# Optimization experiments

Hardware: AMD Instinct MI355X
Metric: run time of the kernel (lower is better)

The kernel has to match this reference:

```python
import jax, jax.numpy as jnp
import numpy as np

B, C, W, H = 8, 256, 64, 64
C8 = C // 8


def setup_inputs() -> dict:
    key = jax.random.key(0)
    ks = jax.random.split(key, 8)
    # xavier_uniform for 1x1 convs: bound = sqrt(6/(fan_in+fan_out))
    def xavier(k, out_c, in_c):
        bound = np.sqrt(6.0 / (in_c + out_c))
        return jax.random.uniform(k, (out_c, in_c), jnp.float32, -bound, bound)
    return {
        "x": jax.random.normal(ks[0], (B, C, W, H), jnp.float32),
        "Wf": xavier(ks[1], C8, C),
        "bf": jnp.zeros((C8,), jnp.float32),
        "Wg": xavier(ks[2], C8, C),
        "bg": jnp.zeros((C8,), jnp.float32),
        "Wh": xavier(ks[3], C, C),
        "bh": jnp.zeros((C,), jnp.float32),
        "gamma": jnp.zeros((1,), jnp.float32),
    }


def reference(x, Wf, bf, Wg, bg, Wh, bh, gamma):
    b, c, w, h = x.shape
    n = w * h
    xf = x.reshape(b, c, n)                                   # (B, C, N)
    # 1x1 convs == per-position channel GEMMs
    f = jnp.einsum('oc,bcn->bon', Wf, xf) + bf[None, :, None]  # (B, C/8, N)
    g = jnp.einsum('oc,bcn->bon', Wg, xf) + bg[None, :, None]  # (B, C/8, N)
    hh = jnp.einsum('oc,bcn->bon', Wh, xf) + bh[None, :, None] # (B, C, N)
    # attention[b,i,j] = softmax_j( f[b,:,i] . g[b,:,j] )
    att = jax.nn.softmax(jnp.einsum('boi,boj->bij', f, g), axis=-1)
    # torch.bmm(h, attention): out[b,c,i] = sum_k h[b,c,k] * att[b,k,i]
    sa = jnp.einsum('bck,bki->bci', hh, att).reshape(b, c, w, h)
    return gamma * sa + x
```

## Files before the change

kernel.cpp:

```cpp
#include <hip/hip_runtime.h>
#include <hip/hip_bf16.h>

#define BB 8
#define CC 256
#define NN 4096
#define LOG2E 1.44269504088896340736f
#define SHIFT 48.0f

typedef __attribute__((ext_vector_type(8))) short short8;
typedef __attribute__((ext_vector_type(4))) float f32x4;

static __device__ __forceinline__ unsigned short f2b(float x) {
  __hip_bfloat16 h = __float2bfloat16(x);
  return *reinterpret_cast<unsigned short*>(&h);
}
static __device__ __forceinline__ unsigned int pk2(float a, float b) {
  return (unsigned int)f2b(a) | ((unsigned int)f2b(b) << 16);
}


__global__ __launch_bounds__(256) void k_wprep(
    const float* __restrict__ Wf, const float* __restrict__ bfv,
    const float* __restrict__ Wg, const float* __restrict__ bgv,
    const float* __restrict__ Wh, const float* __restrict__ bhv,
    unsigned short* __restrict__ wA, float* __restrict__ ball)
{
  const int t = threadIdx.x;
  const int fi = blockIdx.x * 4 + (t >> 6);
  const int l = t & 63;
  const int mg = fi >> 3, kg = fi & 7;
  const int o = mg * 16 + (l & 15);
  const int c0 = kg * 32 + (l >> 4) * 8;
  const float* src; float scale = 1.0f;
  if (o < 32)      { src = Wf + (size_t)o * CC; scale = LOG2E; }
  else if (o < 64) { src = Wg + (size_t)(o - 32) * CC; }
  else             { src = Wh + (size_t)(o - 64) * CC; }
  float4 a = *(const float4*)(src + c0);
  float4 c = *(const float4*)(src + c0 + 4);
  short8 v;
  v[0] = (short)f2b(a.x * scale); v[1] = (short)f2b(a.y * scale);
  v[2] = (short)f2b(a.z * scale); v[3] = (short)f2b(a.w * scale);
  v[4] = (short)f2b(c.x * scale); v[5] = (short)f2b(c.y * scale);
  v[6] = (short)f2b(c.z * scale); v[7] = (short)f2b(c.w * scale);
  *(short8*)(wA + (size_t)fi * 512 + l * 8) = v;
  if (blockIdx.x == 0 && t < 320)
    ball[t] = (t < 32) ? bfv[t] * LOG2E : (t < 64) ? bgv[t - 32] : bhv[t - 64];
}

__global__ __launch_bounds__(512) void k_fgh(
    const float* __restrict__ x, const unsigned short* __restrict__ wA,
    const float* __restrict__ ball,
    unsigned short* __restrict__ fA, unsigned short* __restrict__ gB,
    unsigned short* __restrict__ hA)
{
  __shared__ __align__(16) char smem[41984];
  unsigned short* xb = (unsigned short*)smem;
  unsigned short* TL = (unsigned short*)smem;
  const int bid = blockIdx.x;
  const int b = bid & 7, i0 = (bid >> 3) * 64;
  const int t = threadIdx.x, w = t >> 6, l = t & 63;
  const int ig_w = w & 3, mg0 = (w >> 2) * 10;
  f32x4 acc[10] = {};
  for (int cc = 0; cc < 4; ++cc) {
    __syncthreads();
    {
      short8 v;
      const float* xp = x + ((size_t)b * CC + cc * 64 + w * 8) * NN + i0 + l;
      #pragma unroll
      for (int e = 0; e < 8; ++e) v[e] = (short)f2b(xp[(size_t)e * NN]);
      int frag = (w >> 2) * 4 + (l >> 4);
      int lp = (w & 3) * 16 + (l & 15);
      *(short8*)(xb + (frag * 64 + lp) * 8) = v;
    }
    __syncthreads();
    #pragma unroll
    for (int kg2 = 0; kg2 < 2; ++kg2) {
      short8 bfrag = *(const short8*)(xb + ((kg2 * 4 + ig_w) * 64 + l) * 8);
      int kg = cc * 2 + kg2;
      #pragma unroll
      for (int j = 0; j < 10; ++j) {
        short8 afrag = *(const short8*)(wA +
            ((size_t)((mg0 + j) * 8 + kg)) * 512 + l * 8);
        acc[j] = __builtin_amdgcn_mfma_f32_16x16x32_bf16(afrag, bfrag, acc[j], 0, 0, 0);
      }
    }
  }
  __syncthreads();
  #pragma unroll
  for (int j = 0; j < 10; ++j) {
    int ob = (mg0 + j) * 16 + (l >> 4) * 4;
    float4 bl = *(const float4*)(ball + ob);
    int irow = ig_w * 16 + (l & 15);
    ushort4 pv;
    pv.x = f2b(acc[j][0] + bl.x); pv.y = f2b(acc[j][1] + bl.y);
    pv.z = f2b(acc[j][2] + bl.z); pv.w = f2b(acc[j][3] + bl.w);
    *(ushort4*)(TL + irow * 328 + ob) = pv;
  }
  __syncthreads();
  if (t < 256) {
    int kg_p = t >> 6;
    int o8 = (l >> 4) * 8;
    int irow = kg_p * 16 + (l & 15);
    short8 vf = *(const short8*)(TL + irow * 328 + o8);
    short8 vg = *(const short8*)(TL + irow * 328 + 32 + o8);
    size_t kgG = (size_t)b * 256 + (i0 >> 4) + kg_p;
    *(short8*)(fA + kgG * 512 + l * 8) = vf;
    *(short8*)(gB + kgG * 512 + l * 8) = vg;
  }
  #pragma unroll
  for (int q = 0; q < 4; ++q) {
    int slot = t + q * 512;
    int fr = slot >> 6, ll = slot & 63;
    int cg = fr >> 1, kcl = fr & 1;
    int orow = 64 + cg * 16 + (ll & 15);
    int pbase = kcl * 32 + (ll >> 4) * 8;
    short8 v;
    #pragma unroll
    for (int e = 0; e < 8; ++e) v[e] = (short)TL[(pbase + e) * 328 + orow];
    size_t idx = (((size_t)b * 16 + cg) * 128 + (i0 >> 5) + kcl) * 512 + ll * 8;
    *(short8*)(hA + idx) = v;
  }
}

__global__ __launch_bounds__(512) void k_stats(
    const unsigned short* __restrict__ fA, const unsigned short* __restrict__ gB,
    float* __restrict__ cshift)
{
  __shared__ __align__(16) unsigned short sg[2][16 * 512];
  const int bid = blockIdx.x;
  const int b = bid & 7, kt = bid >> 3;
  const int t = threadIdx.x, w = t >> 6, l = t & 63;
  const int li = l & 15, lh = l >> 4;
  short8 af = *(const short8*)(fA + ((size_t)b * 256 + kt * 8 + w) * 512 + l * 8);
  const unsigned short* gb = gB + (size_t)b * 256 * 512;
  f32x4 zero = {0.f, 0.f, 0.f, 0.f};
  {
    uint4 v0 = *(const uint4*)(gb + ((size_t)(w * 2 + 0) * 64 + l) * 8);
    uint4 v1 = *(const uint4*)(gb + ((size_t)(w * 2 + 1) * 64 + l) * 8);
    *(uint4*)(&sg[0][((w * 2 + 0) * 64 + l) * 8]) = v0;
    *(uint4*)(&sg[0][((w * 2 + 1) * 64 + l) * 8]) = v1;
  }
  __syncthreads();
  float s[4] = {0.f, 0.f, 0.f, 0.f};
  for (int jt = 0; jt < 16; ++jt) {
    if (jt < 15) {
      uint4 v0 = *(const uint4*)(gb + ((size_t)((jt + 1) * 16 + w * 2 + 0) * 64 + l) * 8);
      uint4 v1 = *(const uint4*)(gb + ((size_t)((jt + 1) * 16 + w * 2 + 1) * 64 + l) * 8);
      unsigned short* dst = &sg[(jt + 1) & 1][0];
      *(uint4*)(dst + ((w * 2 + 0) * 64 + l) * 8) = v0;
      *(uint4*)(dst + ((w * 2 + 1) * 64 + l) * 8) = v1;
    }
    const unsigned short* src = &sg[jt & 1][0];
    #pragma unroll
    for (int jf = 0; jf < 16; ++jf) {
      short8 bfrag = *(const short8*)(src + (jf * 64 + l) * 8);
      f32x4 d = __builtin_amdgcn_mfma_f32_16x16x32_bf16(af, bfrag, zero, 0, 0, 0);
      s[0] += exp2f(d[0] - SHIFT);
      s[1] += exp2f(d[1] - SHIFT);
      s[2] += exp2f(d[2] - SHIFT);
      s[3] += exp2f(d[3] - SHIFT);
    }
    __syncthreads();
  }
  #pragma unroll
  for (int mk = 1; mk < 16; mk <<= 1)
    #pragma unroll
    for (int r = 0; r < 4; ++r) s[r] += __shfl_xor(s[r], mk);
  if (li == 0) {
    #pragma unroll
    for (int r = 0; r < 4; ++r) {
      size_t idx = (size_t)b * NN + (kt * 8 + w) * 16 + lh * 4 + r;
      cshift[idx] = SHIFT + log2f(fmaxf(s[r], 1e-30f));
    }
  }
}

__global__ __launch_bounds__(512, 4) void k_out(
    const unsigned short* __restrict__ fA, const unsigned short* __restrict__ gB,
    const unsigned short* __restrict__ hA,
    const float* __restrict__ csv,
    const float* __restrict__ x, const float* __restrict__ gamma,
    float* __restrict__ out)
{
  __shared__ __align__(16) unsigned short pbuf[2 * 16 * 512];
  const int bid = blockIdx.x;
  const int b = bid & 7, i0 = (bid >> 3) * 64;
  const int t = threadIdx.x, w = t >> 6, l = t & 63;
  const int li = l & 15, lh = l >> 4;
  const unsigned short* fAb = fA + ((size_t)b * 256 + w) * 512 + l * 8;
  const unsigned short* hAb = hA + ((size_t)b * 16 + w * 2) * (size_t)128 * 512 + l * 8;
  const float* cs = csv + (size_t)b * NN + w * 16 + lh * 4;
  short8 g[4];
  #pragma unroll
  for (int ig = 0; ig < 4; ++ig)
    g[ig] = *(const short8*)(gB + ((size_t)b * 256 + (i0 >> 4) + ig) * 512 + l * 8);
  const int pl = ((w & 1) * 2 + (lh >> 1)) * 16 + li;
  const int pwo = pl * 8 + (lh & 1) * 4;
  f32x4 zero = {0.f, 0.f, 0.f, 0.f};
  f32x4 acc[2][4] = {};
  short8 afc = *(const short8*)(fAb);
  float4 ccc = *(const float4*)(cs);
  #pragma unroll
  for (int ig = 0; ig < 4; ++ig) {
    f32x4 sfr = __builtin_amdgcn_mfma_f32_16x16x32_bf16(afc, g[ig], zero, 0, 0, 0);
    uint2 v;
    v.x = pk2(exp2f(sfr[0] - ccc.x), exp2f(sfr[1] - ccc.y));
    v.y = pk2(exp2f(sfr[2] - ccc.z), exp2f(sfr[3] - ccc.w));
    *(uint2*)(pbuf + ((size_t)((w >> 1) * 4 + ig)) * 512 + pwo) = v;
  }
  afc = *(const short8*)(fAb + (size_t)8 * 512);
  ccc = *(const float4*)(cs + 128);
  __syncthreads();
  for (int ch = 0; ch < 32; ++ch) {
    unsigned short* pb  = pbuf + (ch & 1) * (16 * 512);
    unsigned short* pnx = pbuf + ((ch + 1) & 1) * (16 * 512);
    short8 hf[8];
    #pragma unroll
    for (int cg = 0; cg < 2; ++cg)
      #pragma unroll
      for (int kb = 0; kb < 4; ++kb)
        hf[cg * 4 + kb] = *(const short8*)(hAb +
            ((size_t)cg * 128 + ch * 4 + kb) * 512);
    if (ch < 31) {
      #pragma unroll
      for (int ig = 0; ig < 4; ++ig) {
        f32x4 sfr = __builtin_amdgcn_mfma_f32_16x16x32_bf16(afc, g[ig], zero, 0, 0, 0);
        uint2 v;
        v.x = pk2(exp2f(sfr[0] - ccc.x), exp2f(sfr[1] - ccc.y));
        v.y = pk2(exp2f(sfr[2] - ccc.z), exp2f(sfr[3] - ccc.w));
        *(uint2*)(pnx + ((size_t)((w >> 1) * 4 + ig)) * 512 + pwo) = v;
      }
      const int ch2 = (ch < 30) ? (ch + 2) : 31;
      afc = *(const short8*)(fAb + (size_t)ch2 * 8 * 512);
      ccc = *(const float4*)(cs + ch2 * 128);
    }
    __builtin_amdgcn_s_setprio(1);
    #pragma unroll
    for (int kb = 0; kb < 4; ++kb)
      #pragma unroll
      for (int ig = 0; ig < 4; ++ig) {
        short8 pf = *(const short8*)(pb + ((kb * 4 + ig) * 64 + l) * 8);
        acc[0][ig] = __builtin_amdgcn_mfma_f32_16x16x32_bf16(pf, hf[kb], acc[0][ig], 0, 0, 0);
        acc[1][ig] = __builtin_amdgcn_mfma_f32_16x16x32_bf16(pf, hf[4 + kb], acc[1][ig], 0, 0, 0);
      }
    __builtin_amdgcn_s_setprio(0);
    __syncthreads();
  }
  const float gm = gamma[0];
  #pragma unroll
  for (int cg = 0; cg < 2; ++cg)
    #pragma unroll
    for (int ig = 0; ig < 4; ++ig) {
      int c = w * 32 + cg * 16 + li;
      int i = i0 + ig * 16 + lh * 4;
      size_t off = ((size_t)b * CC + c) * NN + i;
      float4 xv = *(const float4*)(x + off);
      float4 ov;
      ov.x = gm * acc[cg][ig][0] + xv.x;
      ov.y = gm * acc[cg][ig][1] + xv.y;
      ov.z = gm * acc[cg][ig][2] + xv.z;
      ov.w = gm * acc[cg][ig][3] + xv.w;
      *(float4*)(out + off) = ov;
    }
}

extern "C" void kernel_launch(void* const* d_in, const int* in_sizes, int n_in,
                              void* d_out, int out_size, void* d_ws, size_t ws_size,
                              hipStream_t stream)
{
  const float* x     = (const float*)d_in[0];
  const float* Wf    = (const float*)d_in[1];
  const float* bf    = (const float*)d_in[2];
  const float* Wg    = (const float*)d_in[3];
  const float* bg    = (const float*)d_in[4];
  const float* Wh    = (const float*)d_in[5];
  const float* bh    = (const float*)d_in[6];
  const float* gamma = (const float*)d_in[7];
  float* out = (float*)d_out;

  char* wsb = (char*)d_ws;
  float* cshift = (float*)(wsb + 131072);
  unsigned short* wA = (unsigned short*)(wsb + 262144);
  float* ball        = (float*)(wsb + 425984);
  unsigned short* fA = (unsigned short*)(wsb + 427520);
  unsigned short* gB = (unsigned short*)(wsb + 2524672);
  unsigned short* hA = (unsigned short*)(wsb + 4621824);

  k_wprep<<<40,  256, 0, stream>>>(Wf, bf, Wg, bg, Wh, bh, wA, ball);
  k_fgh  <<<512, 512, 0, stream>>>(x, wA, ball, fA, gB, hA);
  k_stats<<<256, 512, 0, stream>>>(fA, gB, cshift);
  k_out  <<<512, 512, 0, stream>>>(fA, gB, hA, cshift, x, gamma, out);
}
```

Measured before the change: 165.2 us.

## Retile attention-output kernel to 128 query rows per block with full channels per wave

k_out now gives each block 128 query positions instead of 64 and halves the grid to 256 blocks. Each wave owns 16 query columns across all 256 channels, using 16 accumulators, and h fragments are software-prefetched in sub-blocks. The aim is to halve how often each block re-reads the h matrix and recomputes the P tile per query, at the cost of more registers. Dropping the min-blocks hint in launch bounds may lower occupancy, and the smaller grid leaves fewer blocks to spread across CUs.

```diff
diff --git a/kernel.cpp b/kernel.cpp
--- a/kernel.cpp
+++ b/kernel.cpp
@@ -175,7 +175,7 @@
   }
 }
 
-__global__ __launch_bounds__(512, 4) void k_out(
+__global__ __launch_bounds__(512) void k_out(
     const unsigned short* __restrict__ fA, const unsigned short* __restrict__ gB,
     const unsigned short* __restrict__ hA,
     const float* __restrict__ csv,
@@ -184,84 +184,99 @@
 {
   __shared__ __align__(16) unsigned short pbuf[2 * 16 * 512];
   const int bid = blockIdx.x;
-  const int b = bid & 7, i0 = (bid >> 3) * 64;
+  const int b = bid & 7, i0 = (bid >> 3) * 128;
   const int t = threadIdx.x, w = t >> 6, l = t & 63;
   const int li = l & 15, lh = l >> 4;
-  const unsigned short* fAb = fA + ((size_t)b * 256 + w) * 512 + l * 8;
-  const unsigned short* hAb = hA + ((size_t)b * 16 + w * 2) * (size_t)128 * 512 + l * 8;
-  const float* cs = csv + (size_t)b * NN + w * 16 + lh * 4;
-  short8 g[4];
-  #pragma unroll
-  for (int ig = 0; ig < 4; ++ig)
-    g[ig] = *(const short8*)(gB + ((size_t)b * 256 + (i0 >> 4) + ig) * 512 + l * 8);
-  const int pl = ((w & 1) * 2 + (lh >> 1)) * 16 + li;
-  const int pwo = pl * 8 + (lh & 1) * 4;
+  const unsigned short* fAb = fA + (size_t)b * 256 * 512 + l * 8;
+  const unsigned short* hAb = hA + (size_t)b * 16 * 128 * 512 + l * 8;
+  const float* cs = csv + (size_t)b * NN + lh * 4;
+  short8 g = *(const short8*)(gB + ((size_t)b * 256 + (i0 >> 4) + w) * 512 + l * 8);
   f32x4 zero = {0.f, 0.f, 0.f, 0.f};
-  f32x4 acc[2][4] = {};
-  short8 afc = *(const short8*)(fAb);
-  float4 ccc = *(const float4*)(cs);
-  #pragma unroll
-  for (int ig = 0; ig < 4; ++ig) {
-    f32x4 sfr = __builtin_amdgcn_mfma_f32_16x16x32_bf16(afc, g[ig], zero, 0, 0, 0);
+  f32x4 acc[16] = {};
+  short8 afn[4]; float4 ccn[4];
+  #pragma unroll
+  for (int kg = 0; kg < 4; ++kg) {
+    afn[kg] = *(const short8*)(fAb + (size_t)kg * 512);
+    ccn[kg] = *(const float4*)(cs + kg * 16);
+  }
+  #pragma unroll
+  for (int kg = 0; kg < 4; ++kg) {
+    f32x4 s = __builtin_amdgcn_mfma_f32_16x16x32_bf16(afn[kg], g, zero, 0, 0, 0);
     uint2 v;
-    v.x = pk2(exp2f(sfr[0] - ccc.x), exp2f(sfr[1] - ccc.y));
-    v.y = pk2(exp2f(sfr[2] - ccc.z), exp2f(sfr[3] - ccc.w));
-    *(uint2*)(pbuf + ((size_t)((w >> 1) * 4 + ig)) * 512 + pwo) = v;
-  }
-  afc = *(const short8*)(fAb + (size_t)8 * 512);
-  ccc = *(const float4*)(cs + 128);
+    v.x = pk2(exp2f(s[0] - ccn[kg].x), exp2f(s[1] - ccn[kg].y));
+    v.y = pk2(exp2f(s[2] - ccn[kg].z), exp2f(s[3] - ccn[kg].w));
+    int lt = ((kg & 1) * 2 + (lh >> 1)) * 16 + li;
+    *(uint2*)((char*)pbuf + ((w * 2 + (kg >> 1)) * 64 + lt) * 16 + (lh & 1) * 8) = v;
+  }
+  #pragma unroll
+  for (int kg = 0; kg < 4; ++kg) {
+    afn[kg] = *(const short8*)(fAb + (size_t)(4 + kg) * 512);
+    ccn[kg] = *(const float4*)(cs + 64 + kg * 16);
+  }
   __syncthreads();
-  for (int ch = 0; ch < 32; ++ch) {
-    unsigned short* pb  = pbuf + (ch & 1) * (16 * 512);
-    unsigned short* pnx = pbuf + ((ch + 1) & 1) * (16 * 512);
-    short8 hf[8];
-    #pragma unroll
-    for (int cg = 0; cg < 2; ++cg)
-      #pragma unroll
-      for (int kb = 0; kb < 4; ++kb)
-        hf[cg * 4 + kb] = *(const short8*)(hAb +
-            ((size_t)cg * 128 + ch * 4 + kb) * 512);
-    if (ch < 31) {
-      #pragma unroll
-      for (int ig = 0; ig < 4; ++ig) {
-        f32x4 sfr = __builtin_amdgcn_mfma_f32_16x16x32_bf16(afc, g[ig], zero, 0, 0, 0);
+  for (int ch = 0; ch < 64; ++ch) {
+    unsigned short* pb = pbuf + (ch & 1) * 8192;
+    unsigned short* pn = pbuf + ((ch + 1) & 1) * 8192;
+    short8 pA0 = *(const short8*)(pb + ((w * 2 + 0) * 64 + l) * 8);
+    short8 pA1 = *(const short8*)(pb + ((w * 2 + 1) * 64 + l) * 8);
+    short8 hb[8];
+    #pragma unroll
+    for (int q = 0; q < 8; ++q)
+      hb[q] = *(const short8*)(hAb + ((size_t)(q >> 1) * 128 + ch * 2 + (q & 1)) * 512);
+    if (ch < 63) {
+      #pragma unroll
+      for (int kg = 0; kg < 4; ++kg) {
+        f32x4 s = __builtin_amdgcn_mfma_f32_16x16x32_bf16(afn[kg], g, zero, 0, 0, 0);
         uint2 v;
-        v.x = pk2(exp2f(sfr[0] - ccc.x), exp2f(sfr[1] - ccc.y));
-        v.y = pk2(exp2f(sfr[2] - ccc.z), exp2f(sfr[3] - ccc.w));
-        *(uint2*)(pnx + ((size_t)((w >> 1) * 4 + ig)) * 512 + pwo) = v;
-      }
-      const int ch2 = (ch < 30) ? (ch + 2) : 31;
-      afc = *(const short8*)(fAb + (size_t)ch2 * 8 * 512);
-      ccc = *(const float4*)(cs + ch2 * 128);
-    }
-    __builtin_amdgcn_s_setprio(1);
-    #pragma unroll
-    for (int kb = 0; kb < 4; ++kb)
-      #pragma unroll
-      for (int ig = 0; ig < 4; ++ig) {
-        short8 pf = *(const short8*)(pb + ((kb * 4 + ig) * 64 + l) * 8);
-        acc[0][ig] = __builtin_amdgcn_mfma_f32_16x16x32_bf16(pf, hf[kb], acc[0][ig], 0, 0, 0);
-        acc[1][ig] = __builtin_amdgcn_mfma_f32_16x16x32_bf16(pf, hf[4 + kb], acc[1][ig], 0, 0, 0);
-      }
-    __builtin_amdgcn_s_setprio(0);
+        v.x = pk2(exp2f(s[0] - ccn[kg].x), exp2f(s[1] - ccn[kg].y));
+        v.y = pk2(exp2f(s[2] - ccn[kg].z), exp2f(s[3] - ccn[kg].w));
+        int lt = ((kg & 1) * 2 + (lh >> 1)) * 16 + li;
+        *(uint2*)((char*)pn + ((w * 2 + (kg >> 1)) * 64 + lt) * 16 + (lh & 1) * 8) = v;
+      }
+      const int ch2 = (ch < 62) ? (ch + 2) : 63;
+      #pragma unroll
+      for (int kg = 0; kg < 4; ++kg) {
+        afn[kg] = *(const short8*)(fAb + (size_t)(ch2 * 4 + kg) * 512);
+        ccn[kg] = *(const float4*)(cs + ch2 * 64 + kg * 16);
+      }
+    }
+    #pragma unroll
+    for (int sb = 0; sb < 4; ++sb) {
+      short8 hn[8];
+      if (sb < 3) {
+        #pragma unroll
+        for (int q = 0; q < 8; ++q)
+          hn[q] = *(const short8*)(hAb +
+              ((size_t)((sb + 1) * 4 + (q >> 1)) * 128 + ch * 2 + (q & 1)) * 512);
+      }
+      #pragma unroll
+      for (int cgl = 0; cgl < 4; ++cgl) {
+        acc[sb * 4 + cgl] = __builtin_amdgcn_mfma_f32_16x16x32_bf16(
+            pA0, hb[cgl * 2 + 0], acc[sb * 4 + cgl], 0, 0, 0);
+        acc[sb * 4 + cgl] = __builtin_amdgcn_mfma_f32_16x16x32_bf16(
+            pA1, hb[cgl * 2 + 1], acc[sb * 4 + cgl], 0, 0, 0);
+      }
+      if (sb < 3) {
+        #pragma unroll
+        for (int q = 0; q < 8; ++q) hb[q] = hn[q];
+      }
+    }
     __syncthreads();
   }
   const float gm = gamma[0];
   #pragma unroll
-  for (int cg = 0; cg < 2; ++cg)
-    #pragma unroll
-    for (int ig = 0; ig < 4; ++ig) {
-      int c = w * 32 + cg * 16 + li;
-      int i = i0 + ig * 16 + lh * 4;
-      size_t off = ((size_t)b * CC + c) * NN + i;
-      float4 xv = *(const float4*)(x + off);
-      float4 ov;
-      ov.x = gm * acc[cg][ig][0] + xv.x;
-      ov.y = gm * acc[cg][ig][1] + xv.y;
-      ov.z = gm * acc[cg][ig][2] + xv.z;
-      ov.w = gm * acc[cg][ig][3] + xv.w;
-      *(float4*)(out + off) = ov;
-    }
+  for (int cg = 0; cg < 16; ++cg) {
+    int c = cg * 16 + li;
+    int i = i0 + w * 16 + lh * 4;
+    size_t off = ((size_t)b * CC + c) * NN + i;
+    float4 xv = *(const float4*)(x + off);
+    float4 ov;
+    ov.x = gm * acc[cg][0] + xv.x;
+    ov.y = gm * acc[cg][1] + xv.y;
+    ov.z = gm * acc[cg][2] + xv.z;
+    ov.w = gm * acc[cg][3] + xv.w;
+    *(float4*)(out + off) = ov;
+  }
 }
 
 extern "C" void kernel_launch(void* const* d_in, const int* in_sizes, int n_in,
@@ -289,5 +304,5 @@
   k_wprep<<<40,  256, 0, stream>>>(Wf, bf, Wg, bg, Wh, bh, wA, ball);
   k_fgh  <<<512, 512, 0, stream>>>(x, wA, ball, fA, gB, hA);
   k_stats<<<256, 512, 0, stream>>>(fA, gB, cshift);
-  k_out  <<<512, 512, 0, stream>>>(fA, gB, hA, cshift, x, gamma, out);
-}
+  k_out  <<<256, 512, 0, stream>>>(fA, gB, hA, cshift, x, gamma, out);
+}
```

New measurement: 337.9 us. +104.6%, slower.

## Restructure k_out to 4-wave blocks with 64-channel per-wave tiles

Applied to the files above, without the earlier changes.

Shrinks the output kernel from 8 waves to 4 waves per block. Each wave now covers 64 output channels (16 accumulator tiles instead of 8), so each P fragment read from LDS feeds twice as many MFMAs. The key range is split into 64 smaller chunks of 64 keys each. The software pipelining (P computed one chunk ahead, with a sync after the MFMAs) is replaced by compute-then-sync in the same iteration. The gain is more data reuse per wave, paid for with higher register pressure, fewer waves per block, and twice as many barriers with less overlap.

```diff
diff --git a/kernel.cpp b/kernel.cpp
--- a/kernel.cpp
+++ b/kernel.cpp
@@ -175,91 +175,80 @@
   }
 }
 
-__global__ __launch_bounds__(512, 4) void k_out(
+__global__ __launch_bounds__(256) void k_out(
     const unsigned short* __restrict__ fA, const unsigned short* __restrict__ gB,
     const unsigned short* __restrict__ hA,
     const float* __restrict__ csv,
     const float* __restrict__ x, const float* __restrict__ gamma,
     float* __restrict__ out)
 {
-  __shared__ __align__(16) unsigned short pbuf[2 * 16 * 512];
+  __shared__ __align__(16) unsigned short pbuf[2 * 8 * 512];
   const int bid = blockIdx.x;
   const int b = bid & 7, i0 = (bid >> 3) * 64;
   const int t = threadIdx.x, w = t >> 6, l = t & 63;
   const int li = l & 15, lh = l >> 4;
-  const unsigned short* fAb = fA + ((size_t)b * 256 + w) * 512 + l * 8;
-  const unsigned short* hAb = hA + ((size_t)b * 16 + w * 2) * (size_t)128 * 512 + l * 8;
+  const unsigned short* fAb = fA + (size_t)b * 256 * 512 + l * 8;
+  const unsigned short* hAb = hA + ((size_t)b * 16 + w * 4) * (size_t)128 * 512 + l * 8;
   const float* cs = csv + (size_t)b * NN + w * 16 + lh * 4;
   short8 g[4];
   #pragma unroll
   for (int ig = 0; ig < 4; ++ig)
     g[ig] = *(const short8*)(gB + ((size_t)b * 256 + (i0 >> 4) + ig) * 512 + l * 8);
-  const int pl = ((w & 1) * 2 + (lh >> 1)) * 16 + li;
-  const int pwo = pl * 8 + (lh & 1) * 4;
+  const int lt = ((w & 1) * 2 + (lh >> 1)) * 16 + li;
   f32x4 zero = {0.f, 0.f, 0.f, 0.f};
-  f32x4 acc[2][4] = {};
-  short8 afc = *(const short8*)(fAb);
+  f32x4 acc[4][4] = {};
+  short8 afc = *(const short8*)(fAb + (size_t)w * 512);
   float4 ccc = *(const float4*)(cs);
-  #pragma unroll
-  for (int ig = 0; ig < 4; ++ig) {
-    f32x4 sfr = __builtin_amdgcn_mfma_f32_16x16x32_bf16(afc, g[ig], zero, 0, 0, 0);
-    uint2 v;
-    v.x = pk2(exp2f(sfr[0] - ccc.x), exp2f(sfr[1] - ccc.y));
-    v.y = pk2(exp2f(sfr[2] - ccc.z), exp2f(sfr[3] - ccc.w));
-    *(uint2*)(pbuf + ((size_t)((w >> 1) * 4 + ig)) * 512 + pwo) = v;
-  }
-  afc = *(const short8*)(fAb + (size_t)8 * 512);
-  ccc = *(const float4*)(cs + 128);
-  __syncthreads();
-  for (int ch = 0; ch < 32; ++ch) {
-    unsigned short* pb  = pbuf + (ch & 1) * (16 * 512);
-    unsigned short* pnx = pbuf + ((ch + 1) & 1) * (16 * 512);
+  for (int ch = 0; ch < 64; ++ch) {
     short8 hf[8];
     #pragma unroll
-    for (int cg = 0; cg < 2; ++cg)
-      #pragma unroll
-      for (int kb = 0; kb < 4; ++kb)
-        hf[cg * 4 + kb] = *(const short8*)(hAb +
-            ((size_t)cg * 128 + ch * 4 + kb) * 512);
-    if (ch < 31) {
-      #pragma unroll
-      for (int ig = 0; ig < 4; ++ig) {
-        f32x4 sfr = __builtin_amdgcn_mfma_f32_16x16x32_bf16(afc, g[ig], zero, 0, 0, 0);
-        uint2 v;
-        v.x = pk2(exp2f(sfr[0] - ccc.x), exp2f(sfr[1] - ccc.y));
-        v.y = pk2(exp2f(sfr[2] - ccc.z), exp2f(sfr[3] - ccc.w));
-        *(uint2*)(pnx + ((size_t)((w >> 1) * 4 + ig)) * 512 + pwo) = v;
-      }
-      const int ch2 = (ch < 30) ? (ch + 2) : 31;
-      afc = *(const short8*)(fAb + (size_t)ch2 * 8 * 512);
-      ccc = *(const float4*)(cs + ch2 * 128);
-    }
-    __builtin_amdgcn_s_setprio(1);
-    #pragma unroll
-    for (int kb = 0; kb < 4; ++kb)
-      #pragma unroll
-      for (int ig = 0; ig < 4; ++ig) {
-        short8 pf = *(const short8*)(pb + ((kb * 4 + ig) * 64 + l) * 8);
-        acc[0][ig] = __builtin_amdgcn_mfma_f32_16x16x32_bf16(pf, hf[kb], acc[0][ig], 0, 0, 0);
-        acc[1][ig] = __builtin_amdgcn_mfma_f32_16x16x32_bf16(pf, hf[4 + kb], acc[1][ig], 0, 0, 0);
-      }
-    __builtin_amdgcn_s_setprio(0);
-    __syncthreads();
+    for (int cgl = 0; cgl < 4; ++cgl)
+      #pragma unroll
+      for (int ks = 0; ks < 2; ++ks)
+        hf[cgl * 2 + ks] = *(const short8*)(hAb +
+            ((size_t)cgl * 128 + ch * 2 + ks) * 512);
+    unsigned short* pb = pbuf + (ch & 1) * 4096;
+    #pragma unroll
+    for (int ig = 0; ig < 4; ++ig) {
+      f32x4 s = __builtin_amdgcn_mfma_f32_16x16x32_bf16(afc, g[ig], zero, 0, 0, 0);
+      uint2 v;
+      v.x = pk2(exp2f(s[0] - ccc.x), exp2f(s[1] - ccc.y));
+      v.y = pk2(exp2f(s[2] - ccc.z), exp2f(s[3] - ccc.w));
+      *(uint2*)((char*)pb + (((w >> 1) * 4 + ig) * 64 + lt) * 16 + (lh & 1) * 8) = v;
+    }
+    if (ch < 63) {
+      afc = *(const short8*)(fAb + (size_t)((ch + 1) * 4 + w) * 512);
+      ccc = *(const float4*)(cs + (ch + 1) * 64);
+    }
+    __syncthreads();
+    #pragma unroll
+    for (int ks = 0; ks < 2; ++ks) {
+      short8 pf[4];
+      #pragma unroll
+      for (int ig = 0; ig < 4; ++ig)
+        pf[ig] = *(const short8*)(pb + ((ks * 4 + ig) * 64 + l) * 8);
+      #pragma unroll
+      for (int cgl = 0; cgl < 4; ++cgl)
+        #pragma unroll
+        for (int ig = 0; ig < 4; ++ig)
+          acc[cgl][ig] = __builtin_amdgcn_mfma_f32_16x16x32_bf16(
+              pf[ig], hf[cgl * 2 + ks], acc[cgl][ig], 0, 0, 0);
+    }
   }
   const float gm = gamma[0];
   #pragma unroll
-  for (int cg = 0; cg < 2; ++cg)
+  for (int cgl = 0; cgl < 4; ++cgl)
     #pragma unroll
     for (int ig = 0; ig < 4; ++ig) {
-      int c = w * 32 + cg * 16 + li;
+      int c = (w * 4 + cgl) * 16 + li;
       int i = i0 + ig * 16 + lh * 4;
       size_t off = ((size_t)b * CC + c) * NN + i;
       float4 xv = *(const float4*)(x + off);
       float4 ov;
-      ov.x = gm * acc[cg][ig][0] + xv.x;
-      ov.y = gm * acc[cg][ig][1] + xv.y;
-      ov.z = gm * acc[cg][ig][2] + xv.z;
-      ov.w = gm * acc[cg][ig][3] + xv.w;
+      ov.x = gm * acc[cgl][ig][0] + xv.x;
+      ov.y = gm * acc[cgl][ig][1] + xv.y;
+      ov.z = gm * acc[cgl][ig][2] + xv.z;
+      ov.w = gm * acc[cgl][ig][3] + xv.w;
       *(float4*)(out + off) = ov;
     }
 }
@@ -289,5 +278,5 @@
   k_wprep<<<40,  256, 0, stream>>>(Wf, bf, Wg, bg, Wh, bh, wA, ball);
   k_fgh  <<<512, 512, 0, stream>>>(x, wA, ball, fA, gB, hA);
   k_stats<<<256, 512, 0, stream>>>(fA, gB, cshift);
-  k_out  <<<512, 512, 0, stream>>>(fA, gB, hA, cshift, x, gamma, out);
-}
+  k_out  <<<512, 256, 0, stream>>>(fA, gB, hA, cshift, x, gamma, out);
+}
```

Result: slower. 180.0 us (+9.0%).

## Restructure fgh staging layout, dual-accumulate stats, and simplify out-kernel P pipeline

Applied to the files above, without the earlier changes.

In k_fgh, the f/g and h outputs now go to separate shared-memory tiles, with h stored transposed so the h fragment is read as one vector load instead of eight strided scalar loads. In k_stats, the exp-sum uses two independent accumulator sets to shorten the dependency chain. In k_out, the software-pipelined prefetch of the next P chunk and the setprio hints are removed. P is now computed for the current chunk, followed by a single barrier and then the PV MFMAs, with double-buffered pbuf making one barrier per iteration enough. This reduces register pressure and code complexity, but gives up overlap of the exp work with the MFMA work.

```diff
diff --git a/kernel.cpp b/kernel.cpp
--- a/kernel.cpp
+++ b/kernel.cpp
@@ -53,9 +53,10 @@
     unsigned short* __restrict__ fA, unsigned short* __restrict__ gB,
     unsigned short* __restrict__ hA)
 {
-  __shared__ __align__(16) char smem[41984];
+  __shared__ __align__(16) char smem[46080];
   unsigned short* xb = (unsigned short*)smem;
   unsigned short* TL = (unsigned short*)smem;
+  unsigned short* TH = (unsigned short*)(smem + 64 * 72 * 2);
   const int bid = blockIdx.x;
   const int b = bid & 7, i0 = (bid >> 3) * 64;
   const int t = threadIdx.x, w = t >> 6, l = t & 63;
@@ -88,21 +89,32 @@
   __syncthreads();
   #pragma unroll
   for (int j = 0; j < 10; ++j) {
-    int ob = (mg0 + j) * 16 + (l >> 4) * 4;
+    int mg = mg0 + j;
+    int ob = mg * 16 + (l >> 4) * 4;
     float4 bl = *(const float4*)(ball + ob);
     int irow = ig_w * 16 + (l & 15);
-    ushort4 pv;
-    pv.x = f2b(acc[j][0] + bl.x); pv.y = f2b(acc[j][1] + bl.y);
-    pv.z = f2b(acc[j][2] + bl.z); pv.w = f2b(acc[j][3] + bl.w);
-    *(ushort4*)(TL + irow * 328 + ob) = pv;
+    unsigned short q0 = f2b(acc[j][0] + bl.x);
+    unsigned short q1 = f2b(acc[j][1] + bl.y);
+    unsigned short q2 = f2b(acc[j][2] + bl.z);
+    unsigned short q3 = f2b(acc[j][3] + bl.w);
+    if (mg < 4) {
+      ushort4 pv; pv.x = q0; pv.y = q1; pv.z = q2; pv.w = q3;
+      *(ushort4*)(TL + irow * 72 + ob) = pv;
+    } else {
+      int oh = ob - 64;
+      TH[(oh + 0) * 72 + irow] = q0;
+      TH[(oh + 1) * 72 + irow] = q1;
+      TH[(oh + 2) * 72 + irow] = q2;
+      TH[(oh + 3) * 72 + irow] = q3;
+    }
   }
   __syncthreads();
   if (t < 256) {
     int kg_p = t >> 6;
     int o8 = (l >> 4) * 8;
     int irow = kg_p * 16 + (l & 15);
-    short8 vf = *(const short8*)(TL + irow * 328 + o8);
-    short8 vg = *(const short8*)(TL + irow * 328 + 32 + o8);
+    short8 vf = *(const short8*)(TL + irow * 72 + o8);
+    short8 vg = *(const short8*)(TL + irow * 72 + 32 + o8);
     size_t kgG = (size_t)b * 256 + (i0 >> 4) + kg_p;
     *(short8*)(fA + kgG * 512 + l * 8) = vf;
     *(short8*)(gB + kgG * 512 + l * 8) = vg;
@@ -112,11 +124,9 @@
     int slot = t + q * 512;
     int fr = slot >> 6, ll = slot & 63;
     int cg = fr >> 1, kcl = fr & 1;
-    int orow = 64 + cg * 16 + (ll & 15);
+    int orow = cg * 16 + (ll & 15);
     int pbase = kcl * 32 + (ll >> 4) * 8;
-    short8 v;
-    #pragma unroll
-    for (int e = 0; e < 8; ++e) v[e] = (short)TL[(pbase + e) * 328 + orow];
+    short8 v = *(const short8*)(TH + orow * 72 + pbase);
     size_t idx = (((size_t)b * 16 + cg) * 128 + (i0 >> 5) + kcl) * 512 + ll * 8;
     *(short8*)(hA + idx) = v;
   }
@@ -141,7 +151,8 @@
     *(uint4*)(&sg[0][((w * 2 + 1) * 64 + l) * 8]) = v1;
   }
   __syncthreads();
-  float s[4] = {0.f, 0.f, 0.f, 0.f};
+  float s0[4] = {0.f, 0.f, 0.f, 0.f};
+  float s1[4] = {0.f, 0.f, 0.f, 0.f};
   for (int jt = 0; jt < 16; ++jt) {
     if (jt < 15) {
       uint4 v0 = *(const uint4*)(gb + ((size_t)((jt + 1) * 16 + w * 2 + 0) * 64 + l) * 8);
@@ -152,16 +163,22 @@
     }
     const unsigned short* src = &sg[jt & 1][0];
     #pragma unroll
-    for (int jf = 0; jf < 16; ++jf) {
-      short8 bfrag = *(const short8*)(src + (jf * 64 + l) * 8);
-      f32x4 d = __builtin_amdgcn_mfma_f32_16x16x32_bf16(af, bfrag, zero, 0, 0, 0);
-      s[0] += exp2f(d[0] - SHIFT);
-      s[1] += exp2f(d[1] - SHIFT);
-      s[2] += exp2f(d[2] - SHIFT);
-      s[3] += exp2f(d[3] - SHIFT);
-    }
-    __syncthreads();
-  }
+    for (int jf = 0; jf < 16; jf += 2) {
+      short8 bf0 = *(const short8*)(src + ((jf + 0) * 64 + l) * 8);
+      short8 bf1 = *(const short8*)(src + ((jf + 1) * 64 + l) * 8);
+      f32x4 d0 = __builtin_amdgcn_mfma_f32_16x16x32_bf16(af, bf0, zero, 0, 0, 0);
+      f32x4 d1 = __builtin_amdgcn_mfma_f32_16x16x32_bf16(af, bf1, zero, 0, 0, 0);
+      #pragma unroll
+      for (int r = 0; r < 4; ++r) {
+        s0[r] += exp2f(d0[r] - SHIFT);
+        s1[r] += exp2f(d1[r] - SHIFT);
+      }
+    }
+    __syncthreads();
+  }
+  float s[4];
+  #pragma unroll
+  for (int r = 0; r < 4; ++r) s[r] = s0[r] + s1[r];
   #pragma unroll
   for (int mk = 1; mk < 16; mk <<= 1)
     #pragma unroll
@@ -198,22 +215,7 @@
   const int pwo = pl * 8 + (lh & 1) * 4;
   f32x4 zero = {0.f, 0.f, 0.f, 0.f};
   f32x4 acc[2][4] = {};
-  short8 afc = *(const short8*)(fAb);
-  float4 ccc = *(const float4*)(cs);
-  #pragma unroll
-  for (int ig = 0; ig < 4; ++ig) {
-    f32x4 sfr = __builtin_amdgcn_mfma_f32_16x16x32_bf16(afc, g[ig], zero, 0, 0, 0);
-    uint2 v;
-    v.x = pk2(exp2f(sfr[0] - ccc.x), exp2f(sfr[1] - ccc.y));
-    v.y = pk2(exp2f(sfr[2] - ccc.z), exp2f(sfr[3] - ccc.w));
-    *(uint2*)(pbuf + ((size_t)((w >> 1) * 4 + ig)) * 512 + pwo) = v;
-  }
-  afc = *(const short8*)(fAb + (size_t)8 * 512);
-  ccc = *(const float4*)(cs + 128);
-  __syncthreads();
   for (int ch = 0; ch < 32; ++ch) {
-    unsigned short* pb  = pbuf + (ch & 1) * (16 * 512);
-    unsigned short* pnx = pbuf + ((ch + 1) & 1) * (16 * 512);
     short8 hf[8];
     #pragma unroll
     for (int cg = 0; cg < 2; ++cg)
@@ -221,20 +223,18 @@
       for (int kb = 0; kb < 4; ++kb)
         hf[cg * 4 + kb] = *(const short8*)(hAb +
             ((size_t)cg * 128 + ch * 4 + kb) * 512);
-    if (ch < 31) {
-      #pragma unroll
-      for (int ig = 0; ig < 4; ++ig) {
-        f32x4 sfr = __builtin_amdgcn_mfma_f32_16x16x32_bf16(afc, g[ig], zero, 0, 0, 0);
-        uint2 v;
-        v.x = pk2(exp2f(sfr[0] - ccc.x), exp2f(sfr[1] - ccc.y));
-        v.y = pk2(exp2f(sfr[2] - ccc.z), exp2f(sfr[3] - ccc.w));
-        *(uint2*)(pnx + ((size_t)((w >> 1) * 4 + ig)) * 512 + pwo) = v;
-      }
-      const int ch2 = (ch < 30) ? (ch + 2) : 31;
-      afc = *(const short8*)(fAb + (size_t)ch2 * 8 * 512);
-      ccc = *(const float4*)(cs + ch2 * 128);
-    }
-    __builtin_amdgcn_s_setprio(1);
+    short8 af = *(const short8*)(fAb + (size_t)ch * 8 * 512);
+    float4 cc = *(const float4*)(cs + ch * 128);
+    unsigned short* pb = pbuf + (ch & 1) * (16 * 512);
+    #pragma unroll
+    for (int ig = 0; ig < 4; ++ig) {
+      f32x4 sfr = __builtin_amdgcn_mfma_f32_16x16x32_bf16(af, g[ig], zero, 0, 0, 0);
+      uint2 v;
+      v.x = pk2(exp2f(sfr[0] - cc.x), exp2f(sfr[1] - cc.y));
+      v.y = pk2(exp2f(sfr[2] - cc.z), exp2f(sfr[3] - cc.w));
+      *(uint2*)(pb + ((size_t)((w >> 1) * 4 + ig)) * 512 + pwo) = v;
+    }
+    __syncthreads();
     #pragma unroll
     for (int kb = 0; kb < 4; ++kb)
       #pragma unroll
@@ -243,8 +243,6 @@
         acc[0][ig] = __builtin_amdgcn_mfma_f32_16x16x32_bf16(pf, hf[kb], acc[0][ig], 0, 0, 0);
         acc[1][ig] = __builtin_amdgcn_mfma_f32_16x16x32_bf16(pf, hf[4 + kb], acc[1][ig], 0, 0, 0);
       }
-    __builtin_amdgcn_s_setprio(0);
-    __syncthreads();
   }
   const float gm = gamma[0];
   #pragma unroll
```

Result: no change. 165.6 us (+0.3%).
